# Kernel optimization log

Measured on AMD Instinct MI355X. Metric: run time of the kernel, lower is better.

The kernel has to match this reference:

```python
import jax, jax.numpy as jnp
import numpy as np

CHUNK = 256  # rows of the distance matrix materialized at a time


def _min_sq_dist(x, y):
    """For each point in x [N,3], squared distance to nearest point in y [M,3].
    Computed tile-by-tile via lax.scan so the full [N,M] matrix is never built.
    Matches pytorch3d knn_points(K=1).dists (squared Euclidean)."""
    n = x.shape[0]
    x2 = jnp.sum(x * x, axis=-1)            # [N]
    y2 = jnp.sum(y * y, axis=-1)            # [M]
    xs = x.reshape(n // CHUNK, CHUNK, 3)
    x2s = x2.reshape(n // CHUNK, CHUNK)

    def body(carry, inp):
        xc, x2c = inp                        # [C,3], [C]
        d = x2c[:, None] + y2[None, :] - 2.0 * (xc @ y.T)
        return carry, jnp.min(d, axis=1)     # [C]

    _, mins = jax.lax.scan(body, None, (xs, x2s))
    return mins.reshape(-1)                  # [N]


def setup_inputs() -> dict:
    key = jax.random.key(0)
    k1, k2 = jax.random.split(key)
    pred = jax.random.normal(k1, (131072, 4), dtype=jnp.float32)
    target = jax.random.normal(k2, (131072, 4), dtype=jnp.float32)
    return {"pred": pred, "target": target}


def reference(pred, target):
    loss_weight = 1.0
    p = pred[:, :3]
    t = target[:, :3]
    min_p2t = _min_sq_dist(p, t)   # adv_KNN: pred -> target
    min_t2p = _min_sq_dist(t, p)   # ori_KNN: target -> pred
    chamfer = jnp.mean(min_p2t) + jnp.mean(min_t2p)
    return chamfer * loss_weight
```

## Files before the change

kernel.cpp:

```cpp
#include <hip/hip_runtime.h>


#define GF 64
#define GSHF 6
#define CCF (GF * GF * GF)
#define HF 0.1f
#define INVHF 10.0f
#define ORIGF (-3.2f)
#define NCHF (CCF / 256)
#define SSF 262160u

#define G2 32
#define GSH2 5
#define CC2 (G2 * G2 * G2)
#define H2 0.4f
#define INVH2 2.5f
#define ORIG2 (-6.4f)
#define NCH2 (CC2 / 256)
#define SS2 32784u

#define INFB 3.4e38f

__device__ __forceinline__ int cellcoordF(float x) {
    int c = (int)floorf((x - ORIGF) * INVHF);
    return min(max(c, 0), GF - 1);
}
__device__ __forceinline__ int cellofF(float x, float y, float z) {
    return (cellcoordF(z) << (2 * GSHF)) + (cellcoordF(y) << GSHF) + cellcoordF(x);
}
__device__ __forceinline__ int cellcoord2(float x) {
    int c = (int)floorf((x - ORIG2) * INVH2);
    return min(max(c, 0), G2 - 1);
}
__device__ __forceinline__ int cellof2(float x, float y, float z) {
    return (cellcoord2(z) << (2 * GSH2)) + (cellcoord2(y) << GSH2) + cellcoord2(x);
}
__device__ __forceinline__ float axdist2(int u, float qc) {
    float lo = ORIG2 + u * H2;
    float dlo = (u == 0) ? 0.0f : lo - qc;
    float dhi = (u == G2 - 1) ? 0.0f : qc - (lo + H2);
    return fmaxf(0.0f, fmaxf(dlo, dhi));
}
__device__ __forceinline__ float scan_run(
    const float4* __restrict__ pts, unsigned int k, unsigned int ke,
    float cx, float cy, float cz, float lbest) {
    for (; k < ke; ++k) {
        float4 ya = pts[k];
        lbest = fminf(lbest, fmaf(cx, ya.x, fmaf(cy, ya.y, fmaf(cz, ya.z, ya.w))));
    }
    return lbest;
}

__global__ __launch_bounds__(256) void hist2_kernel(
    const float4* __restrict__ A, const float4* __restrict__ B,
    unsigned int* __restrict__ countsF, unsigned int* __restrict__ countsC,
    int n) {
    int i = blockIdx.x * 256 + threadIdx.x;
    const float4* in = blockIdx.y ? B : A;
    unsigned int* cF = countsF + (size_t)blockIdx.y * CCF;
    unsigned int* cC = countsC + (size_t)blockIdx.y * CC2;
    if (i < n) {
        float4 a = in[i];
        atomicAdd(&cF[cellofF(a.x, a.y, a.z)], 1u);
        atomicAdd(&cC[cellof2(a.x, a.y, a.z)], 1u);
    }
}

__global__ __launch_bounds__(256) void scan_chunk_all_kernel(
    const unsigned int* __restrict__ countsF, unsigned int* __restrict__ exclF,
    unsigned int* __restrict__ bsF,
    const unsigned int* __restrict__ countsC, unsigned int* __restrict__ exclC,
    unsigned int* __restrict__ bsC) {
    __shared__ unsigned int lds[256];
    int bid = blockIdx.x;
    const unsigned int* cnt;
    unsigned int* excl;
    unsigned int* bsp;
    int g;
    if (bid < 2 * NCHF) {
        int b = bid >> 10, cb = bid & (NCHF - 1);
        g = cb * 256 + threadIdx.x;
        cnt = countsF + (size_t)b * CCF;
        excl = exclF + (size_t)b * SSF;
        bsp = bsF + bid;
    } else {
        int b2 = bid - 2 * NCHF;
        int b = b2 >> 7, cb = b2 & (NCH2 - 1);
        g = cb * 256 + threadIdx.x;
        cnt = countsC + (size_t)b * CC2;
        excl = exclC + (size_t)b * SS2;
        bsp = bsC + b2;
    }
    unsigned int v = cnt[g];
    lds[threadIdx.x] = v;
    __syncthreads();
    for (int off = 1; off < 256; off <<= 1) {
        unsigned int t = (threadIdx.x >= off) ? lds[threadIdx.x - off] : 0u;
        __syncthreads();
        lds[threadIdx.x] += t;
        __syncthreads();
    }
    excl[g] = lds[threadIdx.x] - v;
    if (threadIdx.x == 255) *bsp = lds[255];
}

__global__ __launch_bounds__(256) void scan_sums_all_kernel(
    unsigned int* __restrict__ bsF, unsigned int* __restrict__ bsC) {
    int b = blockIdx.x;
    unsigned int* bs = (b < 2) ? bsF + b * NCHF : bsC + (b - 2) * NCH2;
    int len = (b < 2) ? NCHF : NCH2;
    __shared__ unsigned int lds[256];
    __shared__ unsigned int carrySh;
    if (threadIdx.x == 0) carrySh = 0;
    __syncthreads();
    for (int base = 0; base < len; base += 256) {
        int idx = base + threadIdx.x;
        unsigned int v = (idx < len) ? bs[idx] : 0u;
        lds[threadIdx.x] = v;
        __syncthreads();
        for (int off = 1; off < 256; off <<= 1) {
            unsigned int t = (threadIdx.x >= off) ? lds[threadIdx.x - off] : 0u;
            __syncthreads();
            lds[threadIdx.x] += t;
            __syncthreads();
        }
        unsigned int carry = carrySh;
        if (idx < len) bs[idx] = carry + lds[threadIdx.x] - v;
        __syncthreads();
        if (threadIdx.x == 255) carrySh = carry + lds[255];
        __syncthreads();
    }
}

__global__ __launch_bounds__(256) void add_offsets_all_kernel(
    unsigned int* __restrict__ exclF, unsigned int* __restrict__ nextF,
    const unsigned int* __restrict__ bsF,
    unsigned int* __restrict__ exclC, unsigned int* __restrict__ nextC,
    const unsigned int* __restrict__ bsC, int n) {
    int bid = blockIdx.x;
    unsigned int* excl;
    unsigned int* next;
    unsigned int add;
    int g, cells;
    if (bid < 2 * NCHF) {
        int b = bid >> 10, cb = bid & (NCHF - 1);
        g = cb * 256 + threadIdx.x;
        excl = exclF + (size_t)b * SSF;
        next = nextF + (size_t)b * CCF;
        add = bsF[bid];
        cells = CCF;
    } else {
        int b2 = bid - 2 * NCHF;
        int b = b2 >> 7, cb = b2 & (NCH2 - 1);
        g = cb * 256 + threadIdx.x;
        excl = exclC + (size_t)b * SS2;
        next = nextC + (size_t)b * CC2;
        add = bsC[b2];
        cells = CC2;
    }
    unsigned int v = excl[g] + add;
    excl[g] = v;
    next[g] = v;
    if (g == 0) excl[cells] = (unsigned int)n;
}

__global__ __launch_bounds__(256) void scatter_all_kernel(
    const float4* __restrict__ A, const float4* __restrict__ B,
    unsigned int* __restrict__ nextF, unsigned int* __restrict__ nextC,
    float4* __restrict__ sortedF, float4* __restrict__ sortedC, int n) {
    int i = blockIdx.x * 256 + threadIdx.x;
    const float4* in = blockIdx.y ? B : A;
    unsigned int* nxF = nextF + (size_t)blockIdx.y * CCF;
    unsigned int* nxC = nextC + (size_t)blockIdx.y * CC2;
    float4* outF = sortedF + (size_t)blockIdx.y * n;
    float4* outC = sortedC + (size_t)blockIdx.y * n;
    if (i < n) {
        float4 a = in[i];
        float s = fmaf(a.x, a.x, fmaf(a.y, a.y, a.z * a.z));
        float4 pt = make_float4(a.x, a.y, a.z, s);
        unsigned int sF = atomicAdd(&nxF[cellofF(a.x, a.y, a.z)], 1u);
        outF[sF] = pt;
        unsigned int sC = atomicAdd(&nxC[cellof2(a.x, a.y, a.z)], 1u);
        outC[sC] = pt;
    }
}

__global__ __launch_bounds__(256) void nn_pass1_kernel(
    const float4* __restrict__ sortedF, const unsigned int* __restrict__ startF,
    int n, unsigned int* __restrict__ wlPT, unsigned int* __restrict__ wbPT,
    unsigned int* __restrict__ cnts, double* __restrict__ acc) {
    int dir = blockIdx.y;
    const float4* Q = sortedF + (size_t)dir * n;
    const float4* pts = sortedF + (size_t)(1 - dir) * n;
    const unsigned int* start = startF + (size_t)(1 - dir) * SSF;
    unsigned int* wl = wlPT + (size_t)dir * n;
    unsigned int* wb = wbPT + (size_t)dir * n;
    unsigned int* cnt = cnts + dir;

    int i = blockIdx.x * 256 + threadIdx.x;
    float v = 0.0f;
    if (i < n) {
        float4 q = Q[i];
        float cx = -2.0f * q.x, cy = -2.0f * q.y, cz = -2.0f * q.z;
        float q2 = q.w;
        int qx = cellcoordF(q.x), qy = cellcoordF(q.y), qz = cellcoordF(q.z);
        int x0 = max(qx - 1, 0), x1 = min(qx + 1, GF - 1);
        unsigned int ss[9], ee[9];
        int idx = 0;
#pragma unroll
        for (int dz = -1; dz <= 1; ++dz) {
            int uz = min(max(qz + dz, 0), GF - 1);
#pragma unroll
            for (int dy = -1; dy <= 1; ++dy) {
                int uy = min(max(qy + dy, 0), GF - 1);
                unsigned int base = ((unsigned)uz << (2 * GSHF)) + ((unsigned)uy << GSHF);
                ss[idx] = start[base + x0];
                ee[idx] = start[base + x1 + 1];
                ++idx;
            }
        }
        float best = INFB;
#pragma unroll
        for (int r = 0; r < 9; ++r) {
            unsigned int k = ss[r], e = ee[r];
            for (; k + 2 <= e; k += 2) {
                float4 ya = pts[k];
                float4 yb = pts[k + 1];
                float ea = fmaf(cx, ya.x, fmaf(cy, ya.y, fmaf(cz, ya.z, ya.w)));
                float eb = fmaf(cx, yb.x, fmaf(cy, yb.y, fmaf(cz, yb.z, yb.w)));
                best = fminf(fminf(best, ea), eb);
            }
            if (k < e) {
                float4 ya = pts[k];
                best = fminf(best, fmaf(cx, ya.x, fmaf(cy, ya.y, fmaf(cz, ya.z, ya.w))));
            }
        }
        float ba = q2 + best;
        float fx = q.x - (ORIGF + (float)qx * HF);
        float fy = q.y - (ORIGF + (float)qy * HF);
        float fz = q.z - (ORIGF + (float)qz * HF);
        float bx = fminf((qx >= 2) ? (fx + HF) : INFB,
                         (qx <= GF - 3) ? (2.0f * HF - fx) : INFB);
        float by = fminf((qy >= 2) ? (fy + HF) : INFB,
                         (qy <= GF - 3) ? (2.0f * HF - fy) : INFB);
        float bz = fminf((qz >= 2) ? (fz + HF) : INFB,
                         (qz <= GF - 3) ? (2.0f * HF - fz) : INFB);
        float bound = fminf(bx, fminf(by, bz)) * 0.99999f;
        if (ba <= bound * bound) {
            v = ba;
        } else {
            unsigned int w = atomicAdd(cnt, 1u);
            wl[w] = (unsigned int)i;
            wb[w] = __float_as_uint(best);
        }
    }
    for (int off = 32; off > 0; off >>= 1) v += __shfl_down(v, off);
    __shared__ float partial[4];
    int lane = threadIdx.x & 63, wid = threadIdx.x >> 6;
    if (lane == 0) partial[wid] = v;
    __syncthreads();
    if (threadIdx.x == 0)
        atomicAdd(acc, (double)((partial[0] + partial[1]) + (partial[2] + partial[3])));
}

__global__ __launch_bounds__(256) void nn_pass2_kernel(
    const float4* __restrict__ sortedF, const float4* __restrict__ sortedC,
    const unsigned int* __restrict__ startC,
    int n, const unsigned int* __restrict__ wlPT, const unsigned int* __restrict__ wbPT,
    const unsigned int* __restrict__ cnts, double* __restrict__ acc) {
    int dir = blockIdx.y;
    const float4* Q = sortedF + (size_t)dir * n;
    const float4* pts = sortedC + (size_t)(1 - dir) * n;
    const unsigned int* start = startC + (size_t)(1 - dir) * SS2;
    const unsigned int* wl = wlPT + (size_t)dir * n;
    const unsigned int* wb = wbPT + (size_t)dir * n;
    unsigned int m = cnts[dir];

    int lane = threadIdx.x & 63;
    int gwave = (blockIdx.x * 256 + threadIdx.x) >> 6;
    int nwave = gridDim.x * 4;
    float wsum = 0.0f;
    for (unsigned int e = gwave; e < m; e += (unsigned int)nwave) {
        unsigned int qi = wl[e];
        float4 q = Q[qi];
        float cx = -2.0f * q.x, cy = -2.0f * q.y, cz = -2.0f * q.z;
        float q2 = q.w;
        int qx = cellcoord2(q.x), qy = cellcoord2(q.y), qz = cellcoord2(q.z);
        float fx = q.x - (ORIG2 + (float)qx * H2);
        float fy = q.y - (ORIG2 + (float)qy * H2);
        float fz = q.z - (ORIG2 + (float)qz * H2);
        float best = __uint_as_float(wb[e]);
        int Rb = 1;
        if (best < INFB) {
            float D = sqrtf(fmaxf(q2 + best, 0.0f));
            Rb = min(max((int)ceilf(D * INVH2), 1), 3);
        }
        int Rp = -1;
        for (;;) {
            int z0 = max(qz - Rb, 0), z1 = min(qz + Rb, G2 - 1);
            int y0 = max(qy - Rb, 0), y1 = min(qy + Rb, G2 - 1);
            int x0 = max(qx - Rb, 0), x1 = min(qx + Rb, G2 - 1);
            int nyr = y1 - y0 + 1;
            int nrows = (z1 - z0 + 1) * nyr;
            float lbest = best;
            for (int r = lane; r < nrows; r += 64) {
                int uz = z0 + r / nyr;
                int uy = y0 + r % nyr;
                int az = uz > qz ? uz - qz : qz - uz;
                int ay = uy > qy ? uy - qy : qy - uy;
                float dz = axdist2(uz, q.z), dy = axdist2(uy, q.y);
                float rowd2 = fmaf(dz, dz, dy * dy);
                if (rowd2 >= q2 + lbest) continue;
                unsigned int base = ((unsigned)uz << (2 * GSH2)) + ((unsigned)uy << GSH2);
                if (az <= Rp && ay <= Rp) {
                    int xa1 = qx - Rp - 1;
                    int xb0 = qx + Rp + 1;
                    if (xa1 >= x0)
                        lbest = scan_run(pts, start[base + x0], start[base + xa1 + 1],
                                         cx, cy, cz, lbest);
                    if (xb0 <= x1)
                        lbest = scan_run(pts, start[base + xb0], start[base + x1 + 1],
                                         cx, cy, cz, lbest);
                } else {
                    lbest = scan_run(pts, start[base + x0], start[base + x1 + 1],
                                     cx, cy, cz, lbest);
                }
            }
            for (int off = 32; off > 0; off >>= 1)
                lbest = fminf(lbest, __shfl_xor(lbest, off));
            best = lbest;
            float bx = fminf((qx - Rb >= 1) ? fmaf((float)Rb, H2, fx) : INFB,
                             (qx + Rb + 1 <= G2 - 1) ? ((float)(Rb + 1) * H2 - fx) : INFB);
            float by = fminf((qy - Rb >= 1) ? fmaf((float)Rb, H2, fy) : INFB,
                             (qy + Rb + 1 <= G2 - 1) ? ((float)(Rb + 1) * H2 - fy) : INFB);
            float bz = fminf((qz - Rb >= 1) ? fmaf((float)Rb, H2, fz) : INFB,
                             (qz + Rb + 1 <= G2 - 1) ? ((float)(Rb + 1) * H2 - fz) : INFB);
            float bound = fminf(bx, fminf(by, bz)) * 0.99999f;
            if (q2 + best <= bound * bound || Rb >= G2) break;
            Rp = Rb;
            Rb = min(Rb + 1, G2);
        }
        wsum += q2 + best;
    }
    if (lane == 0 && wsum != 0.0f) atomicAdd(acc, (double)wsum);
}

__global__ void finalize_kernel(const double* __restrict__ acc,
                                float* __restrict__ out, int n) {
    out[0] = (float)(acc[0] / (double)n);
}

#define SPLIT 16
#define PTS 4
__global__ __launch_bounds__(256) void pack_kernel(
    const float4* __restrict__ in, float4* __restrict__ out, int n) {
    int i = blockIdx.x * 256 + threadIdx.x;
    if (i < n) {
        float4 a = in[i];
        float s = fmaf(a.x, a.x, fmaf(a.y, a.y, a.z * a.z));
        out[i] = make_float4(a.x, a.y, a.z, s);
    }
}
__device__ __forceinline__ unsigned int enc_f32(float f) {
    unsigned int u = __float_as_uint(f);
    return (u & 0x80000000u) ? ~u : (u | 0x80000000u);
}
__device__ __forceinline__ float dec_f32(unsigned int u) {
    u = (u & 0x80000000u) ? (u ^ 0x80000000u) : ~u;
    return __uint_as_float(u);
}
__global__ __launch_bounds__(256) void chamfer_dir_kernel(
    const float4* __restrict__ X, const float4* __restrict__ Y,
    int m, unsigned int* __restrict__ mins) {
    int base = blockIdx.x * (256 * PTS) + threadIdx.x;
    float x2x[PTS], x2y[PTS], x2z[PTS], xw[PTS], mn[PTS];
#pragma unroll
    for (int p = 0; p < PTS; ++p) {
        float4 x = X[base + p * 256];
        x2x[p] = -2.0f * x.x; x2y[p] = -2.0f * x.y; x2z[p] = -2.0f * x.z;
        xw[p] = x.w; mn[p] = INFB;
    }
    int seglen = m / SPLIT, j0 = blockIdx.y * seglen, j1 = j0 + seglen;
    for (int j = j0; j < j1; j += 8) {
#pragma unroll
        for (int u = 0; u < 8; u += 2) {
            float4 ya = Y[j + u];
            float4 yb = Y[j + u + 1];
#pragma unroll
            for (int p = 0; p < PTS; ++p) {
                float ea = fmaf(x2x[p], ya.x, fmaf(x2y[p], ya.y, fmaf(x2z[p], ya.z, ya.w)));
                float eb = fmaf(x2x[p], yb.x, fmaf(x2y[p], yb.y, fmaf(x2z[p], yb.z, yb.w)));
                mn[p] = fminf(fminf(mn[p], ea), eb);
            }
        }
    }
#pragma unroll
    for (int p = 0; p < PTS; ++p)
        atomicMin(&mins[base + p * 256], enc_f32(xw[p] + mn[p]));
}
__global__ __launch_bounds__(256) void reduce_kernel(
    const unsigned int* __restrict__ mins, int total, double* __restrict__ acc) {
    float s = 0.0f;
    for (int i = blockIdx.x * 256 + threadIdx.x; i < total; i += gridDim.x * 256)
        s += dec_f32(mins[i]);
    for (int off = 32; off > 0; off >>= 1) s += __shfl_down(s, off);
    __shared__ float partial[4];
    int lane = threadIdx.x & 63, wid = threadIdx.x >> 6;
    if (lane == 0) partial[wid] = s;
    __syncthreads();
    if (threadIdx.x == 0)
        atomicAdd(acc, (double)((partial[0] + partial[1]) + (partial[2] + partial[3])));
}

extern "C" void kernel_launch(void* const* d_in, const int* in_sizes, int n_in,
                              void* d_out, int out_size, void* d_ws, size_t ws_size,
                              hipStream_t stream) {
    const float4* pred = (const float4*)d_in[0];
    const float4* targ = (const float4*)d_in[1];
    float* out = (float*)d_out;
    int n = in_sizes[0] / 4;
    int nblk = (n + 255) / 256;

    char* ws = (char*)d_ws;
    double* acc = (double*)ws;
    unsigned int* cnts = (unsigned int*)(ws + 8);

    size_t startFB = (size_t)SSF * 4;
    size_t startCB = (size_t)SS2 * 4;
    size_t needGrid = 64 + 2 * startFB + 2 * startCB + 2ull * CCF * 4
                    + 2ull * CC2 * 4 + 4ull * n * 16 + 4ull * n * 4
                    + 2ull * NCHF * 4 + 2ull * NCH2 * 4;

    if (ws_size >= needGrid && n == 131072) {
        char* p = ws + 64;
        unsigned int* startF = (unsigned int*)p;   p += 2 * startFB;
        unsigned int* startC = (unsigned int*)p;   p += 2 * startCB;
        unsigned int* nextF = (unsigned int*)p;    p += 2ull * CCF * 4;
        unsigned int* nextC = (unsigned int*)p;    p += 2ull * CC2 * 4;
        float4* sortedF = (float4*)p;              p += 2ull * n * 16;
        float4* sortedC = (float4*)p;              p += 2ull * n * 16;
        unsigned int* wlPT = (unsigned int*)p;     p += 2ull * n * 4;
        unsigned int* wbPT = (unsigned int*)p;     p += 2ull * n * 4;
        unsigned int* bsF = (unsigned int*)p;      p += 2ull * NCHF * 4;
        unsigned int* bsC = (unsigned int*)p;

        hipMemsetAsync(ws, 0, 64, stream);
        hipMemsetAsync(nextF, 0, 2ull * CCF * 4 + 2ull * CC2 * 4, stream);
        hist2_kernel<<<dim3(nblk, 2), 256, 0, stream>>>(pred, targ, nextF, nextC, n);
        scan_chunk_all_kernel<<<2 * NCHF + 2 * NCH2, 256, 0, stream>>>(
            nextF, startF, bsF, nextC, startC, bsC);
        scan_sums_all_kernel<<<4, 256, 0, stream>>>(bsF, bsC);
        add_offsets_all_kernel<<<2 * NCHF + 2 * NCH2, 256, 0, stream>>>(
            startF, nextF, bsF, startC, nextC, bsC, n);
        scatter_all_kernel<<<dim3(nblk, 2), 256, 0, stream>>>(
            pred, targ, nextF, nextC, sortedF, sortedC, n);

        nn_pass1_kernel<<<dim3(nblk, 2), 256, 0, stream>>>(
            sortedF, startF, n, wlPT, wbPT, cnts, acc);
        nn_pass2_kernel<<<dim3(512, 2), 256, 0, stream>>>(
            sortedF, sortedC, startC, n, wlPT, wbPT, cnts, acc);
    } else {
        hipMemsetAsync(acc, 0, sizeof(double), stream);
        size_t needBF = 64 + 2ull * n * sizeof(float4) + 2ull * n * sizeof(unsigned int);
        if (ws_size >= needBF && (n % (256 * PTS)) == 0 && (n % SPLIT) == 0) {
            float4* P = (float4*)(ws + 64);
            float4* T = P + n;
            unsigned int* minPT = (unsigned int*)(T + n);
            pack_kernel<<<nblk, 256, 0, stream>>>(pred, P, n);
            pack_kernel<<<nblk, 256, 0, stream>>>(targ, T, n);
            hipMemsetAsync(minPT, 0xFF, 2ull * n * sizeof(unsigned int), stream);
            dim3 grid(n / (256 * PTS), SPLIT);
            chamfer_dir_kernel<<<grid, 256, 0, stream>>>(P, T, n, minPT);
            chamfer_dir_kernel<<<grid, 256, 0, stream>>>(T, P, n, minPT + n);
            reduce_kernel<<<256, 256, 0, stream>>>(minPT, 2 * n, acc);
        }
    }
    finalize_kernel<<<1, 1, 0, stream>>>(acc, out, n);
}
```

Baseline: 286.5 us.

## Parallelize pass-2 fallback over points per row with x-range pruning

In the wavefront-per-query fallback pass, the lanes now split the points inside one cell row instead of splitting rows, with a wave-wide min reduction after each row so the best distance tightens immediately. Each row's x-cell range is also clipped to the sphere defined by the current best distance. The grid for pass 2 is doubled. This is meant to fix the load imbalance of one lane scanning a long row serially. In exchange it adds a shuffle reduction per row and serializes the rows.

After: 416.9 us. 45.5% more time.

```diff
diff --git a/kernel.cpp b/kernel.cpp
--- a/kernel.cpp
+++ b/kernel.cpp
@@ -40,15 +40,6 @@
     float dlo = (u == 0) ? 0.0f : lo - qc;
     float dhi = (u == G2 - 1) ? 0.0f : qc - (lo + H2);
     return fmaxf(0.0f, fmaxf(dlo, dhi));
-}
-__device__ __forceinline__ float scan_run(
-    const float4* __restrict__ pts, unsigned int k, unsigned int ke,
-    float cx, float cy, float cz, float lbest) {
-    for (; k < ke; ++k) {
-        float4 ya = pts[k];
-        lbest = fminf(lbest, fmaf(cx, ya.x, fmaf(cy, ya.y, fmaf(cz, ya.z, ya.w))));
-    }
-    return lbest;
 }
 
 __global__ __launch_bounds__(256) void hist2_kernel(
@@ -300,35 +291,59 @@
             int z0 = max(qz - Rb, 0), z1 = min(qz + Rb, G2 - 1);
             int y0 = max(qy - Rb, 0), y1 = min(qy + Rb, G2 - 1);
             int x0 = max(qx - Rb, 0), x1 = min(qx + Rb, G2 - 1);
-            int nyr = y1 - y0 + 1;
-            int nrows = (z1 - z0 + 1) * nyr;
-            float lbest = best;
-            for (int r = lane; r < nrows; r += 64) {
-                int uz = z0 + r / nyr;
-                int uy = y0 + r % nyr;
+            for (int uz = z0; uz <= z1; ++uz) {
+                float dz = axdist2(uz, q.z);
+                float dz2 = dz * dz;
+                if (dz2 >= q2 + best) continue;
                 int az = uz > qz ? uz - qz : qz - uz;
-                int ay = uy > qy ? uy - qy : qy - uy;
-                float dz = axdist2(uz, q.z), dy = axdist2(uy, q.y);
-                float rowd2 = fmaf(dz, dz, dy * dy);
-                if (rowd2 >= q2 + lbest) continue;
-                unsigned int base = ((unsigned)uz << (2 * GSH2)) + ((unsigned)uy << GSH2);
-                if (az <= Rp && ay <= Rp) {
-                    int xa1 = qx - Rp - 1;
-                    int xb0 = qx + Rp + 1;
-                    if (xa1 >= x0)
-                        lbest = scan_run(pts, start[base + x0], start[base + xa1 + 1],
-                                         cx, cy, cz, lbest);
-                    if (xb0 <= x1)
-                        lbest = scan_run(pts, start[base + xb0], start[base + x1 + 1],
-                                         cx, cy, cz, lbest);
-                } else {
-                    lbest = scan_run(pts, start[base + x0], start[base + x1 + 1],
-                                     cx, cy, cz, lbest);
+                unsigned int zb = (unsigned)uz << (2 * GSH2);
+                for (int uy = y0; uy <= y1; ++uy) {
+                    float dy = axdist2(uy, q.y);
+                    float rowd2 = fmaf(dy, dy, dz2);
+                    float rem = q2 + best - rowd2;
+                    if (rem <= 0.0f) continue;
+                    int ay = uy > qy ? uy - qy : qy - uy;
+                    float dxa = sqrtf(fminf(rem, 1.0e8f));
+                    int xl = max(x0, cellcoord2(q.x - dxa));
+                    int xr = min(x1, cellcoord2(q.x + dxa));
+                    if (xl > xr) continue;
+                    unsigned int base = zb + ((unsigned)uy << GSH2);
+                    float lb = best;
+                    if (az <= Rp && ay <= Rp) {
+                        int sa1 = min(xr, qx - Rp - 1);
+                        int sb0 = max(xl, qx + Rp + 1);
+                        if (xl <= sa1) {
+                            unsigned int k0 = start[base + xl];
+                            unsigned int k1 = start[base + sa1 + 1];
+                            for (unsigned int k = k0 + lane; k < k1; k += 64) {
+                                float4 ya = pts[k];
+                                lb = fminf(lb, fmaf(cx, ya.x,
+                                        fmaf(cy, ya.y, fmaf(cz, ya.z, ya.w))));
+                            }
+                        }
+                        if (sb0 <= xr) {
+                            unsigned int k0 = start[base + sb0];
+                            unsigned int k1 = start[base + xr + 1];
+                            for (unsigned int k = k0 + lane; k < k1; k += 64) {
+                                float4 ya = pts[k];
+                                lb = fminf(lb, fmaf(cx, ya.x,
+                                        fmaf(cy, ya.y, fmaf(cz, ya.z, ya.w))));
+                            }
+                        }
+                    } else {
+                        unsigned int k0 = start[base + xl];
+                        unsigned int k1 = start[base + xr + 1];
+                        for (unsigned int k = k0 + lane; k < k1; k += 64) {
+                            float4 ya = pts[k];
+                            lb = fminf(lb, fmaf(cx, ya.x,
+                                    fmaf(cy, ya.y, fmaf(cz, ya.z, ya.w))));
+                        }
+                    }
+                    for (int off = 32; off > 0; off >>= 1)
+                        lb = fminf(lb, __shfl_xor(lb, off));
+                    best = lb;
                 }
             }
-            for (int off = 32; off > 0; off >>= 1)
-                lbest = fminf(lbest, __shfl_xor(lbest, off));
-            best = lbest;
             float bx = fminf((qx - Rb >= 1) ? fmaf((float)Rb, H2, fx) : INFB,
                              (qx + Rb + 1 <= G2 - 1) ? ((float)(Rb + 1) * H2 - fx) : INFB);
             float by = fminf((qy - Rb >= 1) ? fmaf((float)Rb, H2, fy) : INFB,
@@ -457,7 +472,7 @@
 
         nn_pass1_kernel<<<dim3(nblk, 2), 256, 0, stream>>>(
             sortedF, startF, n, wlPT, wbPT, cnts, acc);
-        nn_pass2_kernel<<<dim3(512, 2), 256, 0, stream>>>(
+        nn_pass2_kernel<<<dim3(1024, 2), 256, 0, stream>>>(
             sortedF, sortedC, startC, n, wlPT, wbPT, cnts, acc);
     } else {
         hipMemsetAsync(acc, 0, sizeof(double), stream);
```
